# Optimization experiments

Measured on AMD Instinct MI355X. Metric: run time of the kernel, lower is better.

The kernel has to match this reference:

```python
import jax, jax.numpy as jnp
import numpy as np
from jax import lax

RPN_BBOX_STD_DEV = np.array([0.1, 0.1, 0.2, 0.2], dtype=np.float32)
PRE_NMS_LIMIT = 6000
PROPOSAL_COUNT = 1000
NMS_THRESHOLD = 0.7


def apply_box_deltas(boxes, deltas):
    # boxes: [N,4] (y1,x1,y2,x2); deltas: [N,4] (dy,dx,log dh,log dw)
    h = boxes[:, 2] - boxes[:, 0]
    w = boxes[:, 3] - boxes[:, 1]
    cy = boxes[:, 0] + 0.5 * h + deltas[:, 0] * h
    cx = boxes[:, 1] + 0.5 * w + deltas[:, 1] * w
    h = h * jnp.exp(deltas[:, 2])
    w = w * jnp.exp(deltas[:, 3])
    y1 = cy - 0.5 * h
    x1 = cx - 0.5 * w
    return jnp.stack([y1, x1, y1 + h, x1 + w], axis=1)


def pairwise_iou(boxes):
    # boxes: [N,4] -> iou [N,N]
    y1, x1, y2, x2 = boxes[:, 0], boxes[:, 1], boxes[:, 2], boxes[:, 3]
    area = (y2 - y1) * (x2 - x1)
    iy1 = jnp.maximum(y1[:, None], y1[None, :])
    ix1 = jnp.maximum(x1[:, None], x1[None, :])
    iy2 = jnp.minimum(y2[:, None], y2[None, :])
    ix2 = jnp.minimum(x2[:, None], x2[None, :])
    inter = jnp.maximum(iy2 - iy1, 0.0) * jnp.maximum(ix2 - ix1, 0.0)
    union = area[:, None] + area[None, :] - inter
    return inter / jnp.maximum(union, 1e-12)


def nms_keep_mask(boxes, iou_threshold):
    # boxes are sorted by descending score; greedy suppression.
    n = boxes.shape[0]
    iou = pairwise_iou(boxes)  # [N,N]
    idxs = jnp.arange(n)

    def body(i, keep):
        suppressed = jnp.any((iou[i] > iou_threshold) & keep & (idxs < i))
        return keep.at[i].set(jnp.logical_not(suppressed))

    return lax.fori_loop(0, n, body, jnp.zeros((n,), dtype=bool))


def proposal_single(scores, deltas, anchors):
    # scores: [A], deltas: [A,4], anchors: [A,4] -- single image
    top_scores, ix = lax.top_k(scores, PRE_NMS_LIMIT)           # sorted desc
    d = deltas[ix] * RPN_BBOX_STD_DEV[None, :]
    boxes = apply_box_deltas(anchors[ix], d)
    boxes = jnp.clip(boxes, 0.0, 1.0)                           # window [0,0,1,1]
    keep = lax.stop_gradient(nms_keep_mask(boxes, NMS_THRESHOLD))
    # select top PROPOSAL_COUNT kept boxes in score order, pad with zeros
    masked = jnp.where(keep, top_scores, -jnp.inf)
    _, sel = lax.top_k(masked, PROPOSAL_COUNT)
    valid = keep[sel]
    props = jnp.where(valid[:, None], boxes[sel], 0.0)          # [P,4]
    return props


def reference(rpn_probs, rpn_bbox, anchors):
    scores = rpn_probs[:, :, 1]  # fg prob
    return jax.vmap(proposal_single)(scores, rpn_bbox, anchors)


def setup_inputs() -> dict:
    key = jax.random.key(0)
    k1, k2, k3, k4 = jax.random.split(key, 4)
    B, A = 8, 131072
    rpn_probs = jax.random.uniform(k1, (B, A, 2), dtype=jnp.float32)
    rpn_bbox = jax.random.normal(k2, (B, A, 4), dtype=jnp.float32)
    # valid normalized anchors: y1<y2, x1<x2, inside [0,1]
    tl = jax.random.uniform(k3, (B, A, 2), dtype=jnp.float32) * 0.9
    wh = jax.random.uniform(k4, (B, A, 2), dtype=jnp.float32) * 0.1 + 1e-3
    anchors = jnp.concatenate([tl, tl + wh], axis=-1)
    return {"rpn_probs": rpn_probs, "rpn_bbox": rpn_bbox, "anchors": anchors}
```

## Files before the change

### kernel.cpp

```cpp
#include <hip/hip_runtime.h>

#pragma clang fp contract(off)

typedef unsigned long long u64;
typedef unsigned int u32;
typedef unsigned short u16;

#define BATCH 8
#define NA 131072
#define NSEL 6000
#define NW 94
#define NPAD (NW * 64)
#define CAND_CAP 8192
#define PROP 1000
#define SCAP 1024
#define LDSE 6016
#define CELLCAP 256
#define LARGECAP 1024
#define LTHR 0.125f

#define OFF_HIST     0
#define OFF_BFILL    8256
#define OFF_SCNT     16512
#define OFF_CELLCNT  19584
#define OFF_DIAGT    21696
#define MEMSET_BYTES 406720
#define OFF_CAND     406720
#define OFF_BOXES    931008
#define OFF_CELLLIST 1701056
#define OFF_LARGE    1963200
#define OFF_SENT     1979584

__device__ __forceinline__ int bucket_of(u32 bits) {
  u32 hi = bits >> 16;
  if (hi >= 0x3E80u && hi < 0x3F80u) return (int)(hi - 0x3E80u);
  if (hi >= 0x3F80u && hi < 0x8000u) return 255;
  return -1;
}

__device__ __forceinline__ bool iou_gt(float4 A, float4 B, float areaA, float areaB) {
  float iy = fminf(A.z, B.z) - fmaxf(A.x, B.x);
  float ix = fminf(A.w, B.w) - fmaxf(A.y, B.y);
  float inter = fmaxf(iy, 0.0f) * fmaxf(ix, 0.0f);
  float uni = (areaA + areaB) - inter;
  float uc = fmaxf(uni, 1e-12f);
  return (double)inter >= 0x1.666667p-1 * (double)uc;
}

__device__ __forceinline__ void emit_pair(int b, int ra, int rb, u64* diagT,
                                          u64* sent, int* scnt) {
  int src = min(ra, rb), dst = max(ra, rb);
  int wsrc = src >> 6, wdst = dst >> 6;
  if (wsrc == wdst) {
    atomicOr(&diagT[((size_t)b * NW + wdst) * 64 + (dst & 63)], 1ULL << (src & 63));
  } else {
    int e = atomicAdd(&scnt[b * NW + wsrc], 1);
    if (e < SCAP) {
      u64* p = sent + ((size_t)(b * NW + wsrc) * SCAP + e) * 2;
      p[0] = 1ULL << (dst & 63);
      p[1] = ((u64)(dst >> 6) << 8) | (u64)(src & 63);
    }
  }
}

__device__ __forceinline__ u64 shfl_xor_u64(u64 v, int lanemask) {
  u32 lo = (u32)v, hi = (u32)(v >> 32);
  lo = (u32)__shfl_xor((int)lo, lanemask);
  hi = (u32)__shfl_xor((int)hi, lanemask);
  return ((u64)hi << 32) | (u64)lo;
}

__device__ __forceinline__ void prefix_from_hist(const int* __restrict__ hist, int b,
                                                 int* h, int* bst, int* tb_s) {
  if (threadIdx.x < 256) h[threadIdx.x] = hist[b * 257 + threadIdx.x];
  __syncthreads();
  if (threadIdx.x == 0) {
    int run = 0, t = 0;
    bool found = false;
    for (int v = 255; v >= 0; --v) {
      bst[v] = run;
      run += h[v];
      if (!found && run >= NSEL) { t = v; found = true; }
    }
    *tb_s = t;
  }
  __syncthreads();
}

__global__ __launch_bounds__(256) void hist_kernel(const float* __restrict__ probs,
                                                   int* __restrict__ hist) {
  int b = blockIdx.y;
  const float2* p2 = reinterpret_cast<const float2*>(probs);
  __shared__ int h[257];
  for (int i = threadIdx.x; i < 257; i += 256) h[i] = 0;
  __syncthreads();
  int stride = gridDim.x * blockDim.x;
  for (int a = blockIdx.x * blockDim.x + threadIdx.x; a < NA; a += stride) {
    float sc = p2[(size_t)b * NA + a].y;
    int bk = bucket_of(__float_as_uint(sc));
    atomicAdd(&h[bk < 0 ? 256 : bk], 1);
  }
  __syncthreads();
  for (int i = threadIdx.x; i < 257; i += 256)
    if (h[i]) atomicAdd(&hist[b * 257 + i], h[i]);
}

__global__ __launch_bounds__(256) void gather_kernel(const float* __restrict__ probs,
                                                     const int* __restrict__ hist,
                                                     int* __restrict__ bfill,
                                                     u64* __restrict__ cand) {
  int b = blockIdx.y;
  const float2* p2 = reinterpret_cast<const float2*>(probs);
  __shared__ int h[256];
  __shared__ int bst[256];
  __shared__ int tb_s;
  prefix_from_hist(hist, b, h, bst, &tb_s);
  int tb = tb_s;
  int stride = gridDim.x * blockDim.x;
  for (int a = blockIdx.x * blockDim.x + threadIdx.x; a < NA; a += stride) {
    float sc = p2[(size_t)b * NA + a].y;
    u32 bits = __float_as_uint(sc);
    int bk = bucket_of(bits);
    if (bk >= tb) {
      int pos = bst[bk] + atomicAdd(&bfill[b * 257 + bk], 1);
      if (pos < CAND_CAP)
        cand[(size_t)b * CAND_CAP + pos] = ((u64)bits << 32) | (u64)(0xFFFFFFFFu - (u32)a);
    }
  }
}

__global__ __launch_bounds__(256) void sortdecode_kernel(const int* __restrict__ hist,
                                                         const int* __restrict__ bfill,
                                                         const u64* __restrict__ cand,
                                                         const float* __restrict__ anchors,
                                                         const float* __restrict__ deltas,
                                                         float4* __restrict__ boxes,
                                                         int* __restrict__ cellCnt,
                                                         u16* __restrict__ cellList,
                                                         u16* __restrict__ largeList) {
  int b = blockIdx.y;
  int tid = threadIdx.x;
  __shared__ int h[256];
  __shared__ int bst[256];
  __shared__ int tb_s;
  prefix_from_hist(hist, b, h, bst, &tb_s);
  if (blockIdx.x == 0) {
    float4 z = {0.f, 0.f, 0.f, 0.f};
    for (int r = NSEL + tid; r < NPAD; r += 256) boxes[(size_t)b * NPAD + r] = z;
  }
  int v = tb_s + blockIdx.x;
  if (v > 255) return;
  int start = bst[v];
  if (start >= NSEL) return;
  int cnt = min(min(bfill[b * 257 + v], 1024), CAND_CAP - start);
  if (cnt <= 0) return;
  const u64* seg = cand + (size_t)b * CAND_CAP + start;
  __shared__ u64 s[1024];
  u64 x[4];
#pragma unroll
  for (int p = 0; p < 4; ++p) {
    int i = p * 256 + tid;
    x[p] = (i < cnt) ? seg[i] : 0ULL;
  }
  for (int k = 2; k <= 64; k <<= 1) {
    for (int j = k >> 1; j >= 1; j >>= 1) {
#pragma unroll
      for (int p = 0; p < 4; ++p) {
        int i = p * 256 + tid;
        u64 pv = shfl_xor_u64(x[p], j);
        bool takemax = (((i & j) == 0) == ((i & k) == 0));
        u64 mx = x[p] > pv ? x[p] : pv;
        u64 mn = x[p] < pv ? x[p] : pv;
        x[p] = takemax ? mx : mn;
      }
    }
  }
#pragma unroll
  for (int p = 0; p < 4; ++p) s[p * 256 + tid] = x[p];
  __syncthreads();
  for (int k = 128; k <= 1024; k <<= 1) {
    for (int j = k >> 1; j >= 64; j >>= 1) {
      for (int q = tid; q < 512; q += 256) {
        int i = ((q & ~(j - 1)) << 1) | (q & (j - 1));
        int ixj = i | j;
        u64 a = s[i], c = s[ixj];
        bool up = ((i & k) == 0);
        if (up ? (a < c) : (a > c)) { s[i] = c; s[ixj] = a; }
      }
      __syncthreads();
    }
#pragma unroll
    for (int p = 0; p < 4; ++p) x[p] = s[p * 256 + tid];
    for (int j = 32; j >= 1; j >>= 1) {
#pragma unroll
      for (int p = 0; p < 4; ++p) {
        int i = p * 256 + tid;
        u64 pv = shfl_xor_u64(x[p], j);
        bool takemax = (((i & j) == 0) == ((i & k) == 0));
        u64 mx = x[p] > pv ? x[p] : pv;
        u64 mn = x[p] < pv ? x[p] : pv;
        x[p] = takemax ? mx : mn;
      }
    }
    __syncthreads();
#pragma unroll
    for (int p = 0; p < 4; ++p) s[p * 256 + tid] = x[p];
    __syncthreads();
  }
  for (int i = tid; i < cnt; i += 256) {
    int r = start + i;
    if (r >= NSEL) continue;
    u64 key = s[i];
    float4 o = {0.f, 0.f, 0.f, 0.f};
    u32 idx = 0xFFFFFFFFu - (u32)(key & 0xFFFFFFFFu);
    if (idx < NA) {
      float4 av = *reinterpret_cast<const float4*>(anchors + ((size_t)b * NA + idx) * 4);
      float4 dv = *reinterpret_cast<const float4*>(deltas + ((size_t)b * NA + idx) * 4);
      float y1 = av.x, x1 = av.y, y2 = av.z, x2 = av.w;
      float dy = dv.x * 0.1f, dx = dv.y * 0.1f;
      float dh = dv.z * 0.2f, dw = dv.w * 0.2f;
      float hh = y2 - y1, ww = x2 - x1;
      float cy = y1 + 0.5f * hh + dy * hh;
      float cx = x1 + 0.5f * ww + dx * ww;
      hh = hh * expf(dh);
      ww = ww * expf(dw);
      float ny1 = cy - 0.5f * hh, nx1 = cx - 0.5f * ww;
      float ny2 = ny1 + hh, nx2 = nx1 + ww;
      o.x = fminf(fmaxf(ny1, 0.f), 1.f);
      o.y = fminf(fmaxf(nx1, 0.f), 1.f);
      o.z = fminf(fmaxf(ny2, 0.f), 1.f);
      o.w = fminf(fmaxf(nx2, 0.f), 1.f);
    }
    boxes[(size_t)b * NPAD + r] = o;
    float bh = o.z - o.x, bw = o.w - o.y;
    if (bh > LTHR || bw > LTHR) {
      int pos = atomicAdd(&cellCnt[b * 65 + 64], 1);
      if (pos < LARGECAP) largeList[b * LARGECAP + pos] = (u16)r;
    } else {
      int gy = min(7, max(0, (int)((o.x + o.z) * 4.0f)));
      int gx = min(7, max(0, (int)((o.y + o.w) * 4.0f)));
      int cell = gy * 8 + gx;
      int pos = atomicAdd(&cellCnt[b * 65 + cell], 1);
      if (pos < CELLCAP) cellList[((size_t)b * 64 + cell) * CELLCAP + pos] = (u16)r;
    }
  }
}

__global__ __launch_bounds__(256) void pairs_kernel(const float4* __restrict__ boxes,
                                                    const u16* __restrict__ cellList,
                                                    const u16* __restrict__ largeList,
                                                    const int* __restrict__ cellCnt,
                                                    u64* __restrict__ diagT,
                                                    u64* __restrict__ sent,
                                                    int* __restrict__ scnt) {
  int b = blockIdx.y;
  int tid = threadIdx.x;
  if (blockIdx.x >= 64) {
    int lb = blockIdx.x - 64;
    int nL = min(cellCnt[b * 65 + 64], LARGECAP);
    if (nL == 0) return;
    for (int li = lb; li < nL; li += 64) {
      int L = largeList[b * LARGECAP + li];
      float4 Lb = boxes[(size_t)b * NPAD + L];
      float hL = Lb.z - Lb.x, wL = Lb.w - Lb.y;
      if (0.7f * hL >= 0.126f || 0.7f * wL >= 0.126f) continue;
      float La = hL * wL;
      float sLy = Lb.x + Lb.z, sLx = Lb.y + Lb.w;
      int gy0 = max(0, (int)((sLy - 0.08f) * 4.0f));
      int gy1 = min(7, (int)((sLy + 0.08f) * 4.0f));
      int gx0 = max(0, (int)((sLx - 0.08f) * 4.0f));
      int gx1 = min(7, (int)((sLx + 0.08f) * 4.0f));
      for (int gy = gy0; gy <= gy1; ++gy)
        for (int gx = gx0; gx <= gx1; ++gx) {
          int cc = gy * 8 + gx;
          int cnt = min(cellCnt[b * 65 + cc], CELLCAP);
          for (int i = tid; i < cnt; i += 256) {
            int r = cellList[((size_t)b * 64 + cc) * CELLCAP + i];
            float4 jb = boxes[(size_t)b * NPAD + r];
            float ja = (jb.z - jb.x) * (jb.w - jb.y);
            if (iou_gt(Lb, jb, La, ja)) emit_pair(b, L, r, diagT, sent, scnt);
          }
        }
    }
    int s = 1;
    while ((1 << s) < nL) ++s;
    int tot = nL << s, m = (1 << s) - 1;
    int stride = 64 * 256;
    for (int t = lb * 256 + tid; t < tot; t += stride) {
      int i = t >> s, j = t & m;
      if (j >= nL || i >= j) continue;
      int Li = largeList[b * LARGECAP + i];
      int Lj = largeList[b * LARGECAP + j];
      float4 A = boxes[(size_t)b * NPAD + Li];
      float4 B = boxes[(size_t)b * NPAD + Lj];
      float aA = (A.z - A.x) * (A.w - A.y);
      float aB = (B.z - B.x) * (B.w - B.y);
      if (iou_gt(A, B, aA, aB)) emit_pair(b, Li, Lj, diagT, sent, scnt);
    }
    return;
  }
  int c = blockIdx.x;
  int cy = c >> 3, cx = c & 7;
  int nA = min(cellCnt[b * 65 + c], CELLCAP);
  if (nA == 0) return;
  __shared__ float4 Ab[CELLCAP];
  __shared__ float Aa[CELLCAP];
  __shared__ float Asx[CELLCAP];
  __shared__ float Asy[CELLCAP];
  __shared__ u16 Ai[CELLCAP];
  __shared__ u16 fAi[CELLCAP];
  __shared__ float4 Bb[3 * CELLCAP];
  __shared__ float Ba[3 * CELLCAP];
  __shared__ u16 Bi[3 * CELLCAP];
  __shared__ int nfA_s, nfB_s;
  for (int i = tid; i < nA; i += 256) {
    int r = cellList[((size_t)b * 64 + c) * CELLCAP + i];
    float4 bx = boxes[(size_t)b * NPAD + r];
    Ab[i] = bx;
    Aa[i] = (bx.z - bx.x) * (bx.w - bx.y);
    Asy[i] = bx.x + bx.z;
    Asx[i] = bx.y + bx.w;
    Ai[i] = (u16)r;
  }
  __syncthreads();
  {
    int totS = (nA * (nA - 1)) >> 1;
    for (int t = tid; t < totS; t += 256) {
      int i = (int)((1.0f + sqrtf(8.0f * (float)t + 1.0f)) * 0.5f);
      int tri = (i * (i - 1)) >> 1;
      if (t < tri) {
        --i;
        tri = (i * (i - 1)) >> 1;
      } else if (t >= tri + i) {
        tri += i;
        ++i;
      }
      int j = t - tri;
      if (iou_gt(Ab[i], Ab[j], Aa[i], Aa[j]))
        emit_pair(b, Ai[i], Ai[j], diagT, sent, scnt);
    }
  }
  if (cx < 7) {
    __syncthreads();
    if (tid == 0) { nfA_s = 0; nfB_s = 0; }
    __syncthreads();
    float XR2 = (float)(cx + 1) * 0.25f;
    for (int i = tid; i < nA; i += 256)
      if (Asx[i] > XR2 - 0.078f) fAi[atomicAdd(&nfA_s, 1)] = (u16)i;
    int nc = c + 1;
    int nN = min(cellCnt[b * 65 + nc], CELLCAP);
    for (int i = tid; i < nN; i += 256) {
      int r = cellList[((size_t)b * 64 + nc) * CELLCAP + i];
      float4 bx = boxes[(size_t)b * NPAD + r];
      if (bx.y + bx.w < XR2 + 0.078f) {
        int p = atomicAdd(&nfB_s, 1);
        Bb[p] = bx;
        Ba[p] = (bx.z - bx.x) * (bx.w - bx.y);
        Bi[p] = (u16)r;
      }
    }
    __syncthreads();
    int nfA = nfA_s, nfB = nfB_s;
    if (nfA && nfB) {
      int s = 1;
      while ((1 << s) < nfB) ++s;
      int tot = nfA << s, m = (1 << s) - 1;
      for (int t = tid; t < tot; t += 256) {
        int ii = fAi[t >> s], j = t & m;
        if (j < nfB && iou_gt(Ab[ii], Bb[j], Aa[ii], Ba[j]))
          emit_pair(b, Ai[ii], Bi[j], diagT, sent, scnt);
      }
    }
  }
  if (cy < 7) {
    __syncthreads();
    if (tid == 0) { nfA_s = 0; nfB_s = 0; }
    __syncthreads();
    float YB2 = (float)(cy + 1) * 0.25f;
    float XL2 = (float)cx * 0.25f;
    float XR2 = (float)(cx + 1) * 0.25f;
    for (int i = tid; i < nA; i += 256)
      if (Asy[i] > YB2 - 0.078f) fAi[atomicAdd(&nfA_s, 1)] = (u16)i;
    for (int k = 0; k < 3; ++k) {
      int nx = cx + k - 1;
      if (nx < 0 || nx > 7) continue;
      int nc = (cy + 1) * 8 + nx;
      int nN = min(cellCnt[b * 65 + nc], CELLCAP);
      for (int i = tid; i < nN; i += 256) {
        int r = cellList[((size_t)b * 64 + nc) * CELLCAP + i];
        float4 bx = boxes[(size_t)b * NPAD + r];
        float bsy = bx.x + bx.z, bsx = bx.y + bx.w;
        bool ok = bsy < YB2 + 0.078f;
        if (k == 0) ok = ok && (bsx > XL2 - 0.078f);
        if (k == 2) ok = ok && (bsx < XR2 + 0.078f);
        if (ok) {
          int p = atomicAdd(&nfB_s, 1);
          Bb[p] = bx;
          Ba[p] = (bx.z - bx.x) * (bx.w - bx.y);
          Bi[p] = (u16)r;
        }
      }
    }
    __syncthreads();
    int nfA = nfA_s, nfB = nfB_s;
    if (nfA && nfB) {
      int s = 1;
      while ((1 << s) < nfB) ++s;
      int tot = nfA << s, m = (1 << s) - 1;
      for (int t = tid; t < tot; t += 256) {
        int ii = fAi[t >> s], j = t & m;
        if (j < nfB && iou_gt(Ab[ii], Bb[j], Aa[ii], Ba[j]))
          emit_pair(b, Ai[ii], Bi[j], diagT, sent, scnt);
      }
    }
  }
}

__global__ __launch_bounds__(1024) void nms_kernel(const u64* __restrict__ sent,
                                                   const int* __restrict__ scnt,
                                                   const u64* __restrict__ diagT,
                                                   const float4* __restrict__ boxes,
                                                   float4* __restrict__ out) {
  int b = blockIdx.x;
  int tid = threadIdx.x;
  int lane = tid & 63;
  int wv = tid >> 6;
  __shared__ u64 diag_s[NW * 64];
  __shared__ u64 remv[NW];
  __shared__ u64 ebits[LDSE];
  __shared__ u32 emeta[LDSE];
  __shared__ int cw[NW];
  __shared__ int prefix[NW + 1];
  __shared__ u64 Kw[NW];
  __shared__ int baseW[NW];
  for (int i = tid; i < NW * 64; i += 1024)
    diag_s[i] = diagT[(size_t)b * NW * 64 + i];
  if (tid < NW) {
    remv[tid] = 0ULL;
    cw[tid] = min(scnt[b * NW + tid], SCAP);
  }
  {
    float4 z = {0.f, 0.f, 0.f, 0.f};
    for (int i = tid; i < PROP; i += 1024) out[(size_t)b * PROP + i] = z;
  }
  __syncthreads();
  if (tid == 0) {
    int run = 0;
    for (int w = 0; w < NW; ++w) { prefix[w] = run; run += cw[w]; }
    prefix[NW] = run;
  }
  __syncthreads();
  for (int w = wv; w < NW; w += 16) {
    const u64* gb = sent + (size_t)(b * NW + w) * SCAP * 2;
    int base = prefix[w], n = cw[w];
    for (int e = lane; e < n; e += 64) {
      int slot = base + e;
      if (slot < LDSE) {
        ebits[slot] = gb[e * 2];
        emeta[slot] = (u32)gb[e * 2 + 1];
      }
    }
  }
  __syncthreads();
  if (wv == 0) {
    int total = 0;
    u64 cmask = diag_s[lane];
    for (int w = 0; w < NW; ++w) {
      u64 cmask_next = (w + 1 < NW) ? diag_s[(w + 1) * 64 + lane] : 0ULL;
      u64 rm = remv[w];
      u64 validm = (w * 64 + 64 <= NSEL) ? ~0ULL : ((1ULL << (NSEL - w * 64)) - 1ULL);
      u64 A0 = ~rm & validm;
      bool alive0 = (A0 >> lane) & 1ULL;
      u64 K = __ballot(alive0);
      for (int it = 0; it < 70; ++it) {
        bool alive = alive0 && ((K & cmask) == 0ULL);
        u64 Kn = __ballot(alive);
        if (Kn == K) break;
        K = Kn;
      }
      if (lane == 0) {
        Kw[w] = K;
        baseW[w] = total;
      }
      total += __popcll(K);
      int base = prefix[w], n = cw[w];
      for (int e = lane; e < n; e += 64) {
        int slot = base + e;
        u64 bits;
        u32 meta;
        if (slot < LDSE) {
          bits = ebits[slot];
          meta = emeta[slot];
        } else {
          const u64* ge = sent + ((size_t)(b * NW + w) * SCAP + e) * 2;
          bits = ge[0];
          meta = (u32)ge[1];
        }
        int bb = (int)(meta & 255u);
        int fw = (int)(meta >> 8);
        if ((K >> bb) & 1ULL) atomicOr(&remv[fw], bits);
      }
      cmask = cmask_next;
    }
  }
  __syncthreads();
  for (int i = tid; i < NSEL; i += 1024) {
    int w = i >> 6, bb = i & 63;
    u64 K = Kw[w];
    if ((K >> bb) & 1ULL) {
      int rank = baseW[w] + __popcll(K & ((1ULL << bb) - 1ULL));
      if (rank < PROP) out[(size_t)b * PROP + rank] = boxes[(size_t)b * NPAD + i];
    }
  }
}

extern "C" void kernel_launch(void* const* d_in, const int* in_sizes, int n_in,
                              void* d_out, int out_size, void* d_ws, size_t ws_size,
                              hipStream_t stream) {
  const float* probs = (const float*)d_in[0];
  const float* deltas = (const float*)d_in[1];
  const float* anchors = (const float*)d_in[2];
  char* ws = (char*)d_ws;
  int* hist = (int*)(ws + OFF_HIST);
  int* bfill = (int*)(ws + OFF_BFILL);
  int* scnt = (int*)(ws + OFF_SCNT);
  int* cellCnt = (int*)(ws + OFF_CELLCNT);
  u64* diagT = (u64*)(ws + OFF_DIAGT);
  u64* cand = (u64*)(ws + OFF_CAND);
  float4* boxes = (float4*)(ws + OFF_BOXES);
  u16* cellList = (u16*)(ws + OFF_CELLLIST);
  u16* largeList = (u16*)(ws + OFF_LARGE);
  u64* sent = (u64*)(ws + OFF_SENT);

  (void)hipMemsetAsync(ws, 0, MEMSET_BYTES, stream);

  hist_kernel<<<dim3(64, BATCH), 256, 0, stream>>>(probs, hist);
  gather_kernel<<<dim3(64, BATCH), 256, 0, stream>>>(probs, hist, bfill, cand);
  sortdecode_kernel<<<dim3(64, BATCH), 256, 0, stream>>>(hist, bfill, cand, anchors,
                                                         deltas, boxes, cellCnt,
                                                         cellList, largeList);
  pairs_kernel<<<dim3(128, BATCH), 256, 0, stream>>>(boxes, cellList, largeList,
                                                     cellCnt, diagT, sent, scnt);
  nms_kernel<<<BATCH, 1024, 0, stream>>>(sent, scnt, diagT, boxes, (float4*)d_out);
}
```

Measured before the change: 231.3 us.

## Bucket suppression edges by destination word and pull-resolve them in NMS

Off-diagonal suppression edges are now stored as packed 32-bit entries grouped by destination word instead of source word. The serial NMS wave resolves each word's incoming edges by looking up already-final keep masks before its fixed-point loop, which removes the shared atomicOr push after each word. The next word's first edge batch is prefetched. The diagT zeroing moves from the host memset into sortdecode, shrinking the memset, and the per-word edge capacity is doubled.

```diff
diff --git a/kernel.cpp b/kernel.cpp
--- a/kernel.cpp
+++ b/kernel.cpp
@@ -13,8 +13,8 @@
 #define NPAD (NW * 64)
 #define CAND_CAP 8192
 #define PROP 1000
-#define SCAP 1024
-#define LDSE 6016
+#define SCAP 2048
+#define LDSE 12288
 #define CELLCAP 256
 #define LARGECAP 1024
 #define LTHR 0.125f
@@ -23,8 +23,8 @@
 #define OFF_BFILL    8256
 #define OFF_SCNT     16512
 #define OFF_CELLCNT  19584
+#define MEMSET_BYTES 21696
 #define OFF_DIAGT    21696
-#define MEMSET_BYTES 406720
 #define OFF_CAND     406720
 #define OFF_BOXES    931008
 #define OFF_CELLLIST 1701056
@@ -48,18 +48,15 @@
 }
 
 __device__ __forceinline__ void emit_pair(int b, int ra, int rb, u64* diagT,
-                                          u64* sent, int* scnt) {
+                                          u32* sent, int* scnt) {
   int src = min(ra, rb), dst = max(ra, rb);
   int wsrc = src >> 6, wdst = dst >> 6;
   if (wsrc == wdst) {
     atomicOr(&diagT[((size_t)b * NW + wdst) * 64 + (dst & 63)], 1ULL << (src & 63));
   } else {
-    int e = atomicAdd(&scnt[b * NW + wsrc], 1);
-    if (e < SCAP) {
-      u64* p = sent + ((size_t)(b * NW + wsrc) * SCAP + e) * 2;
-      p[0] = 1ULL << (dst & 63);
-      p[1] = ((u64)(dst >> 6) << 8) | (u64)(src & 63);
-    }
+    int e = atomicAdd(&scnt[b * NW + wdst], 1);
+    if (e < SCAP)
+      sent[(size_t)(b * NW + wdst) * SCAP + e] = ((u32)src << 6) | (u32)(dst & 63);
   }
 }
 
@@ -137,9 +134,14 @@
                                                          float4* __restrict__ boxes,
                                                          int* __restrict__ cellCnt,
                                                          u16* __restrict__ cellList,
-                                                         u16* __restrict__ largeList) {
+                                                         u16* __restrict__ largeList,
+                                                         u64* __restrict__ diagT) {
   int b = blockIdx.y;
   int tid = threadIdx.x;
+  {
+    int g = blockIdx.x * 256 + tid;
+    if (g < NW * 64) diagT[(size_t)b * NW * 64 + g] = 0ULL;
+  }
   __shared__ int h[256];
   __shared__ int bst[256];
   __shared__ int tb_s;
@@ -251,7 +253,7 @@
                                                     const u16* __restrict__ largeList,
                                                     const int* __restrict__ cellCnt,
                                                     u64* __restrict__ diagT,
-                                                    u64* __restrict__ sent,
+                                                    u32* __restrict__ sent,
                                                     int* __restrict__ scnt) {
   int b = blockIdx.y;
   int tid = threadIdx.x;
@@ -416,7 +418,7 @@
   }
 }
 
-__global__ __launch_bounds__(1024) void nms_kernel(const u64* __restrict__ sent,
+__global__ __launch_bounds__(1024) void nms_kernel(const u32* __restrict__ sent,
                                                    const int* __restrict__ scnt,
                                                    const u64* __restrict__ diagT,
                                                    const float4* __restrict__ boxes,
@@ -426,19 +428,17 @@
   int lane = tid & 63;
   int wv = tid >> 6;
   __shared__ u64 diag_s[NW * 64];
-  __shared__ u64 remv[NW];
-  __shared__ u64 ebits[LDSE];
-  __shared__ u32 emeta[LDSE];
+  __shared__ u32 entS[LDSE];
+  __shared__ u32 rmb[NW * 64];
   __shared__ int cw[NW];
   __shared__ int prefix[NW + 1];
-  __shared__ u64 Kw[NW];
+  __shared__ u64 Kw_s[NW];
   __shared__ int baseW[NW];
-  for (int i = tid; i < NW * 64; i += 1024)
+  for (int i = tid; i < NW * 64; i += 1024) {
     diag_s[i] = diagT[(size_t)b * NW * 64 + i];
-  if (tid < NW) {
-    remv[tid] = 0ULL;
-    cw[tid] = min(scnt[b * NW + tid], SCAP);
-  }
+    rmb[i] = 0u;
+  }
+  if (tid < NW) cw[tid] = min(scnt[b * NW + tid], SCAP);
   {
     float4 z = {0.f, 0.f, 0.f, 0.f};
     for (int i = tid; i < PROP; i += 1024) out[(size_t)b * PROP + i] = z;
@@ -451,26 +451,48 @@
   }
   __syncthreads();
   for (int w = wv; w < NW; w += 16) {
-    const u64* gb = sent + (size_t)(b * NW + w) * SCAP * 2;
+    const u32* gb = sent + (size_t)(b * NW + w) * SCAP;
     int base = prefix[w], n = cw[w];
     for (int e = lane; e < n; e += 64) {
       int slot = base + e;
-      if (slot < LDSE) {
-        ebits[slot] = gb[e * 2];
-        emeta[slot] = (u32)gb[e * 2 + 1];
-      }
+      if (slot < LDSE) entS[slot] = gb[e];
     }
   }
   __syncthreads();
   if (wv == 0) {
     int total = 0;
     u64 cmask = diag_s[lane];
+    u32 entp = 0;
+    {
+      int n0 = cw[0];
+      if (lane < n0) {
+        int slot = prefix[0] + lane;
+        entp = (slot < LDSE) ? entS[slot] : sent[(size_t)(b * NW) * SCAP + lane];
+      }
+    }
     for (int w = 0; w < NW; ++w) {
       u64 cmask_next = (w + 1 < NW) ? diag_s[(w + 1) * 64 + lane] : 0ULL;
-      u64 rm = remv[w];
+      int n = cw[w], base = prefix[w];
+      u32 entn = 0;
+      int nn = (w + 1 < NW) ? cw[w + 1] : 0;
+      if (lane < nn) {
+        int slot = prefix[w + 1] + lane;
+        entn = (slot < LDSE) ? entS[slot]
+                             : sent[(size_t)(b * NW + w + 1) * SCAP + lane];
+      }
+      if (lane < n) {
+        int srcr = (int)(entp >> 6);
+        if ((Kw_s[srcr >> 6] >> (srcr & 63)) & 1ULL) rmb[w * 64 + (entp & 63)] = 1u;
+      }
+      for (int e = lane + 64; e < n; e += 64) {
+        int slot = base + e;
+        u32 ent = (slot < LDSE) ? entS[slot] : sent[(size_t)(b * NW + w) * SCAP + e];
+        int srcr = (int)(ent >> 6);
+        if ((Kw_s[srcr >> 6] >> (srcr & 63)) & 1ULL) rmb[w * 64 + (ent & 63)] = 1u;
+      }
+      u32 rb = rmb[w * 64 + lane];
       u64 validm = (w * 64 + 64 <= NSEL) ? ~0ULL : ((1ULL << (NSEL - w * 64)) - 1ULL);
-      u64 A0 = ~rm & validm;
-      bool alive0 = (A0 >> lane) & 1ULL;
+      bool alive0 = (rb == 0u) && ((validm >> lane) & 1ULL);
       u64 K = __ballot(alive0);
       for (int it = 0; it < 70; ++it) {
         bool alive = alive0 && ((K & cmask) == 0ULL);
@@ -479,34 +501,18 @@
         K = Kn;
       }
       if (lane == 0) {
-        Kw[w] = K;
+        Kw_s[w] = K;
         baseW[w] = total;
       }
       total += __popcll(K);
-      int base = prefix[w], n = cw[w];
-      for (int e = lane; e < n; e += 64) {
-        int slot = base + e;
-        u64 bits;
-        u32 meta;
-        if (slot < LDSE) {
-          bits = ebits[slot];
-          meta = emeta[slot];
-        } else {
-          const u64* ge = sent + ((size_t)(b * NW + w) * SCAP + e) * 2;
-          bits = ge[0];
-          meta = (u32)ge[1];
-        }
-        int bb = (int)(meta & 255u);
-        int fw = (int)(meta >> 8);
-        if ((K >> bb) & 1ULL) atomicOr(&remv[fw], bits);
-      }
       cmask = cmask_next;
+      entp = entn;
     }
   }
   __syncthreads();
   for (int i = tid; i < NSEL; i += 1024) {
     int w = i >> 6, bb = i & 63;
-    u64 K = Kw[w];
+    u64 K = Kw_s[w];
     if ((K >> bb) & 1ULL) {
       int rank = baseW[w] + __popcll(K & ((1ULL << bb) - 1ULL));
       if (rank < PROP) out[(size_t)b * PROP + rank] = boxes[(size_t)b * NPAD + i];
@@ -530,7 +536,7 @@
   float4* boxes = (float4*)(ws + OFF_BOXES);
   u16* cellList = (u16*)(ws + OFF_CELLLIST);
   u16* largeList = (u16*)(ws + OFF_LARGE);
-  u64* sent = (u64*)(ws + OFF_SENT);
+  u32* sent = (u32*)(ws + OFF_SENT);
 
   (void)hipMemsetAsync(ws, 0, MEMSET_BYTES, stream);
 
@@ -538,7 +544,7 @@
   gather_kernel<<<dim3(64, BATCH), 256, 0, stream>>>(probs, hist, bfill, cand);
   sortdecode_kernel<<<dim3(64, BATCH), 256, 0, stream>>>(hist, bfill, cand, anchors,
                                                          deltas, boxes, cellCnt,
-                                                         cellList, largeList);
+                                                         cellList, largeList, diagT);
   pairs_kernel<<<dim3(128, BATCH), 256, 0, stream>>>(boxes, cellList, largeList,
                                                      cellCnt, diagT, sent, scnt);
   nms_kernel<<<BATCH, 1024, 0, stream>>>(sent, scnt, diagT, boxes, (float4*)d_out);
```

Result: no change. 234.6 us (+1.4%).
